# Kernel optimization log

Measured on AMD Instinct MI355X. Metric: run time of the kernel, lower is better.

## Reference

```python
import jax, jax.numpy as jnp
import numpy as np

EPS = 1e-12  # torch F.normalize eps
K = 32       # num_clusters (hardcoded in module)

def l2norm(v, axis):
    n = jnp.sqrt(jnp.sum(v * v, axis=axis, keepdims=True))
    return v / jnp.maximum(n, EPS)

def setup_inputs() -> dict:
    key = jax.random.key(0)
    k1, k2, k3, k4 = jax.random.split(key, 4)
    B, M, D = 64, 128, 2048
    x = jax.random.normal(k1, (B, M, D), dtype=jnp.float32)
    # ragged lengths in [1, M]
    lengths = jax.random.randint(k2, (B,), 0, M, dtype=jnp.int32) + 1
    init_sc = 1.0 / np.sqrt(D)
    W = init_sc * jax.random.normal(k3, (K, D), dtype=jnp.float32)  # fc1.weight
    C = init_sc * jax.random.normal(k4, (K, D), dtype=jnp.float32)  # centroids
    return {"x": x, "lengths": lengths, "W": W, "C": C}

def reference(x, lengths, W, C):
    # x: [B,M,D] padded frames, lengths: [B] valid frame counts
    B, M, D = x.shape
    mask = (jnp.arange(M)[None, :] < lengths[:, None]).astype(x.dtype)  # [B,M]
    cnt = lengths.astype(x.dtype)[:, None]                              # [B,1]
    # avg pooling over valid (raw, un-normalized) frames
    avgpool = jnp.sum(x * mask[:, :, None], axis=1) / cnt               # [B,D]
    # per-frame L2 normalize
    xn = l2norm(x, axis=-1)                                             # [B,M,D]
    # soft assignment: linear (no bias) + softmax over clusters
    logits = jnp.einsum('bmd,kd->bmk', xn, W)
    a = jax.nn.softmax(logits, axis=-1) * mask[:, :, None]              # [B,M,K]
    # VLAD residual aggregation, GEMM form:
    # sum_m a[b,m,k]*(xn[b,m,:] - C[k,:]) = (a^T xn) - C * sum_m a
    ax = jnp.einsum('bmk,bmd->bkd', a, xn)                              # [B,K,D]
    asum = jnp.sum(a, axis=1)                                           # [B,K]
    vlad = ax - asum[:, :, None] * C[None, :, :]                        # [B,K,D]
    # intra-normalize per cluster, flatten, global L2 normalize
    vlad = l2norm(vlad, axis=2)
    vlad = vlad.reshape(B, K * D)
    vlad = l2norm(vlad, axis=1)
    return jnp.concatenate([avgpool, vlad], axis=1)                     # [B, D + K*D]
```

## Files before the change

### kernel.cpp

```cpp
#include <hip/hip_runtime.h>
#include <math.h>

#define BB 64
#define MM 128
#define DDIM 2048
#define KK 32
#define NDC 16
#define OUTROW (DDIM + KK*DDIM)

typedef __attribute__((ext_vector_type(8))) short bf16x8;
typedef __attribute__((ext_vector_type(4))) float f32x4;

__device__ __forceinline__ short f2bf(float f) {
  unsigned u = __builtin_bit_cast(unsigned, f);
  u += 0x7fffu + ((u >> 16) & 1u);
  return (short)(u >> 16);
}
__device__ __forceinline__ unsigned pack2(float lo, float hi) {
  return (unsigned)(unsigned short)f2bf(lo) | ((unsigned)(unsigned short)f2bf(hi) << 16);
}

__global__ __launch_bounds__(256) void k_prep(const float* __restrict__ W,
                                              short* __restrict__ Wb) {
  int i = (blockIdx.x * 256 + threadIdx.x) * 8;
  float4 a = *(const float4*)(W + i);
  float4 b = *(const float4*)(W + i + 4);
  bf16x8 o = {f2bf(a.x), f2bf(a.y), f2bf(a.z), f2bf(a.w),
              f2bf(b.x), f2bf(b.y), f2bf(b.z), f2bf(b.w)};
  *(bf16x8*)(Wb + i) = o;
}

__global__ __launch_bounds__(256, 4) void k_logits(const float* __restrict__ x,
    const int* __restrict__ lengths, const short* __restrict__ Wb,
    short* __restrict__ aT, float* __restrict__ asum_p) {
  const int t = threadIdx.x, wv = t >> 6, lane = t & 63;
  const int l15 = lane & 15, quad = lane >> 4;
  const int fg = blockIdx.x;
  const int g0 = fg * 16;
  const int b  = fg >> 3;
  const int m0 = (fg & 7) * 16;
  const int len = lengths[b];

  if (m0 >= len) {
    if (t < KK) asum_p[(size_t)fg * KK + t] = 0.f;
    const int zk = t >> 3, zoff = (t & 7) * 2;
    *(unsigned*)(aT + (size_t)b * KK * MM + (size_t)zk * MM + m0 + zoff) = 0u;
    return;
  }

  const bool av = (m0 + l15) < len;
  const float* xrow = x + (size_t)(g0 + l15) * DDIM + wv * 512 + quad * 8;
  const short* w0   = Wb + l15 * DDIM + wv * 512 + quad * 8;
  const short* w1   = w0 + 16 * DDIM;

  f32x4 c0 = {0.f, 0.f, 0.f, 0.f}, c1 = {0.f, 0.f, 0.f, 0.f};
  float ssq = 0.f;
  #pragma unroll
  for (int h = 0; h < 4; ++h) {
    float4 xa[4], xc[4];
    bf16x8 B0[4], B1[4];
    #pragma unroll
    for (int s = 0; s < 4; ++s) {
      const int so = h * 4 + s;
      if (av) {
        xa[s] = *(const float4*)(xrow + so * 32);
        xc[s] = *(const float4*)(xrow + so * 32 + 4);
      } else {
        xa[s] = make_float4(0.f, 0.f, 0.f, 0.f);
        xc[s] = make_float4(0.f, 0.f, 0.f, 0.f);
      }
      B0[s] = *(const bf16x8*)(w0 + so * 32);
      B1[s] = *(const bf16x8*)(w1 + so * 32);
    }
    #pragma unroll
    for (int s = 0; s < 4; ++s) {
      ssq = fmaf(xa[s].x, xa[s].x, ssq); ssq = fmaf(xa[s].y, xa[s].y, ssq);
      ssq = fmaf(xa[s].z, xa[s].z, ssq); ssq = fmaf(xa[s].w, xa[s].w, ssq);
      ssq = fmaf(xc[s].x, xc[s].x, ssq); ssq = fmaf(xc[s].y, xc[s].y, ssq);
      ssq = fmaf(xc[s].z, xc[s].z, ssq); ssq = fmaf(xc[s].w, xc[s].w, ssq);
      bf16x8 A = {f2bf(xa[s].x), f2bf(xa[s].y), f2bf(xa[s].z), f2bf(xa[s].w),
                  f2bf(xc[s].x), f2bf(xc[s].y), f2bf(xc[s].z), f2bf(xc[s].w)};
      c0 = __builtin_amdgcn_mfma_f32_16x16x32_bf16(A, B0[s], c0, 0, 0, 0);
      c1 = __builtin_amdgcn_mfma_f32_16x16x32_bf16(A, B1[s], c1, 0, 0, 0);
    }
  }

  ssq += __shfl_xor(ssq, 16, 64);
  ssq += __shfl_xor(ssq, 32, 64);
  __shared__ float sq[4][16];
  __shared__ float lg[4][16][33];
  if (quad == 0) sq[wv][l15] = ssq;
  #pragma unroll
  for (int r = 0; r < 4; ++r) {
    lg[wv][quad * 4 + r][l15]      = c0[r];
    lg[wv][quad * 4 + r][16 + l15] = c1[r];
  }
  __syncthreads();

  const int fr = t >> 4, kk = (t & 15) * 2;
  float s0 = 0.f, s1 = 0.f;
  #pragma unroll
  for (int w = 0; w < 4; ++w) { s0 += lg[w][fr][kk]; s1 += lg[w][fr][kk + 1]; }
  float ss  = sq[0][fr] + sq[1][fr] + sq[2][fr] + sq[3][fr];
  float inv = 1.f / fmaxf(sqrtf(ss), 1e-12f);
  s0 *= inv; s1 *= inv;
  float mx = fmaxf(s0, s1);
  mx = fmaxf(mx, __shfl_xor(mx, 1, 64));
  mx = fmaxf(mx, __shfl_xor(mx, 2, 64));
  mx = fmaxf(mx, __shfl_xor(mx, 4, 64));
  mx = fmaxf(mx, __shfl_xor(mx, 8, 64));
  float e0 = __expf(s0 - mx), e1 = __expf(s1 - mx);
  float se = e0 + e1;
  se += __shfl_xor(se, 1, 64);
  se += __shfl_xor(se, 2, 64);
  se += __shfl_xor(se, 4, 64);
  se += __shfl_xor(se, 8, 64);
  const bool valid = (m0 + fr) < len;
  float rr = valid ? (1.f / se) : 0.f;
  float a0 = e0 * rr, a1 = e1 * rr;

  __syncthreads();
  lg[0][fr][kk] = a0; lg[0][fr][kk + 1] = a1;
  __syncthreads();
  if (t < KK) {
    float s = 0.f;
    #pragma unroll
    for (int f = 0; f < 16; ++f) s += lg[0][f][t];
    asum_p[(size_t)fg * KK + t] = s;
  }
  short* ap = aT + (size_t)b * KK * MM + m0 + fr;
  ap[(size_t)kk * MM]       = f2bf(a0 * inv);
  ap[(size_t)(kk + 1) * MM] = f2bf(a1 * inv);
}

__global__ __launch_bounds__(256, 4) void k_vlad(const float* __restrict__ x,
    const int* __restrict__ lengths, const float* __restrict__ Cc,
    const short* __restrict__ aT, const float* __restrict__ asum_p,
    float* __restrict__ out, float* __restrict__ ssq_part) {
  const int t = threadIdx.x, wv = t >> 6, lane = t & 63;
  const int l15 = lane & 15, quad = lane >> 4;
  const int dc = blockIdx.x, b = blockIdx.y;
  const int dh = wv & 1, mh = wv >> 1;
  const int dwb = dc * 128 + dh * 64;
  const int mb  = mh * 64;
  const int len = lengths[b];

  __shared__ __attribute__((aligned(16))) char ubuf[20480];
  short (*xbt)[64][40]     = (short(*)[64][40])ubuf;
  float (*exch)[2][64][20] = (float(*)[2][64][20])ubuf;
  __shared__ float  asl[KK];
  __shared__ float4 avp[2][16];
  __shared__ float  ssw[4][17];

  if (t < KK) {
    float s = 0.f;
    #pragma unroll
    for (int p = 0; p < 8; ++p) s += asum_p[(size_t)(b * 8 + p) * KK + t];
    asl[t] = s;
  }

  const float* xb  = x  + (size_t)b * MM * DDIM;
  const short* at0 = aT + (size_t)b * KK * MM + l15 * MM + mb + quad * 8;

  const int q4   = l15 * 4;
  const int mrow = quad * 2;
  const int keyw = l15 & 3;
  const int keyr = (l15 >> 2) & 3;

  bf16x8 A0[2], A1[2];
  #pragma unroll
  for (int ms = 0; ms < 2; ++ms) {
    A0[ms] = *(const bf16x8*)(at0 + ms * 32);
    A1[ms] = *(const bf16x8*)(at0 + 16 * MM + ms * 32);
  }

  float4 v0[8], v1[8];
  #pragma unroll
  for (int ms = 0; ms < 2; ++ms) {
    #pragma unroll
    for (int p = 0; p < 4; ++p) {
      const int m = mb + ms * 32 + p * 8 + mrow;
      const float* xr = xb + (size_t)m * DDIM + dwb + q4;
      v0[ms * 4 + p] = (m < len) ? *(const float4*)xr
                                 : make_float4(0.f, 0.f, 0.f, 0.f);
      v1[ms * 4 + p] = (m + 1 < len) ? *(const float4*)(xr + DDIM)
                                     : make_float4(0.f, 0.f, 0.f, 0.f);
    }
  }

  float avg[4] = {0.f, 0.f, 0.f, 0.f};
  #pragma unroll
  for (int i = 0; i < 8; ++i) {
    avg[0] += v0[i].x + v1[i].x;
    avg[1] += v0[i].y + v1[i].y;
    avg[2] += v0[i].z + v1[i].z;
    avg[3] += v0[i].w + v1[i].w;
  }
  #pragma unroll
  for (int c = 0; c < 4; ++c) {
    avg[c] += __shfl_xor(avg[c], 16, 64);
    avg[c] += __shfl_xor(avg[c], 32, 64);
  }
  if (mh == 1 && quad == 0)
    avp[dh][l15] = make_float4(avg[0], avg[1], avg[2], avg[3]);

  f32x4 acc0[4], acc1[4];
  #pragma unroll
  for (int nt = 0; nt < 4; ++nt) {
    acc0[nt] = (f32x4){0.f, 0.f, 0.f, 0.f};
    acc1[nt] = (f32x4){0.f, 0.f, 0.f, 0.f};
  }

  #pragma unroll
  for (int ms = 0; ms < 2; ++ms) {
    #pragma unroll
    for (int p = 0; p < 4; ++p) {
      const int i = ms * 4 + p;
      const int mls = (p ^ keyw) * 8 + mrow;
      *(unsigned*)&xbt[wv][q4 + 0][mls] = pack2(v0[i].x, v1[i].x);
      *(unsigned*)&xbt[wv][q4 + 1][mls] = pack2(v0[i].y, v1[i].y);
      *(unsigned*)&xbt[wv][q4 + 2][mls] = pack2(v0[i].z, v1[i].z);
      *(unsigned*)&xbt[wv][q4 + 3][mls] = pack2(v0[i].w, v1[i].w);
    }
    #pragma unroll
    for (int nt = 0; nt < 4; ++nt) {
      bf16x8 B = *(const bf16x8*)&xbt[wv][nt * 16 + l15][(quad ^ keyr) * 8];
      acc0[nt] = __builtin_amdgcn_mfma_f32_16x16x32_bf16(A0[ms], B, acc0[nt], 0, 0, 0);
      acc1[nt] = __builtin_amdgcn_mfma_f32_16x16x32_bf16(A1[ms], B, acc1[nt], 0, 0, 0);
    }
  }

  f32x4 keep[4], give[4];
  if (mh == 0) {
    #pragma unroll
    for (int nt = 0; nt < 4; ++nt) { keep[nt] = acc0[nt]; give[nt] = acc1[nt]; }
  } else {
    #pragma unroll
    for (int nt = 0; nt < 4; ++nt) { keep[nt] = acc1[nt]; give[nt] = acc0[nt]; }
  }

  __syncthreads();
  #pragma unroll
  for (int nt = 0; nt < 4; ++nt)
    *(f32x4*)&exch[dh][mh][lane][nt * 4] = give[nt];

  if (mh == 0 && quad == 0) {
    float4 pa = avp[dh][l15];
    float rl = 1.f / (float)len;
    *(float4*)(out + (size_t)b * OUTROW + dwb + q4) =
        make_float4((avg[0] + pa.x) * rl, (avg[1] + pa.y) * rl,
                    (avg[2] + pa.z) * rl, (avg[3] + pa.w) * rl);
  }

  __syncthreads();
  #pragma unroll
  for (int nt = 0; nt < 4; ++nt)
    keep[nt] += *(const f32x4*)&exch[dh][1 - mh][lane][nt * 4];

  float* orow = out + (size_t)b * OUTROW + DDIM;
  #pragma unroll
  for (int r = 0; r < 4; ++r) {
    const int k = mh * 16 + quad * 4 + r;
    const float as = asl[k];
    float sqv = 0.f;
    #pragma unroll
    for (int nt = 0; nt < 4; ++nt) {
      const int d = dwb + nt * 16 + l15;
      float v = keep[nt][r] - as * Cc[(size_t)k * DDIM + d];
      orow[(size_t)k * DDIM + d] = v;
      sqv = fmaf(v, v, sqv);
    }
    sqv += __shfl_xor(sqv, 1, 64);
    sqv += __shfl_xor(sqv, 2, 64);
    sqv += __shfl_xor(sqv, 4, 64);
    sqv += __shfl_xor(sqv, 8, 64);
    if (l15 == 0) ssw[wv][quad * 4 + r] = sqv;
  }
  __syncthreads();
  if (t < KK) {
    const int mt = t >> 4, kl = t & 15;
    ssq_part[((size_t)dc * BB + b) * KK + t] = ssw[mt * 2][kl] + ssw[mt * 2 + 1][kl];
  }
}

__global__ __launch_bounds__(256) void k_norm(const float* __restrict__ ssq_part,
    float* __restrict__ out) {
  const int t = threadIdx.x;
  const int k = blockIdx.x;
  const int b = blockIdx.y;
  __shared__ float ssk[32];
  if (t < 32) {
    float sk = 0.f;
    #pragma unroll
    for (int dc = 0; dc < NDC; ++dc)
      sk += ssq_part[((size_t)dc * BB + b) * KK + t];
    ssk[t] = sk;
  }
  __syncthreads();
  float gss = 0.f, iv_own = 0.f;
  #pragma unroll
  for (int kk = 0; kk < 32; ++kk) {
    float nk = sqrtf(ssk[kk]);
    float iv = 1.f / fmaxf(nk, 1e-12f);
    float nn = nk * iv;
    gss += nn * nn;
    if (kk == k) iv_own = iv;
  }
  float sc = iv_own / fmaxf(sqrtf(gss), 1e-12f);
  float* row = out + (size_t)b * OUTROW + DDIM + (size_t)k * DDIM;
  #pragma unroll
  for (int h = 0; h < 2; ++h) {
    float4* p = (float4*)(row + h * 1024 + t * 4);
    float4 v = *p;
    v.x *= sc; v.y *= sc; v.z *= sc; v.w *= sc;
    *p = v;
  }
}

extern "C" void kernel_launch(void* const* d_in, const int* in_sizes, int n_in,
                              void* d_out, int out_size, void* d_ws, size_t ws_size,
                              hipStream_t stream) {
  const float* x       = (const float*)d_in[0];
  const int*   lengths = (const int*)d_in[1];
  const float* W       = (const float*)d_in[2];
  const float* C       = (const float*)d_in[3];
  float* out = (float*)d_out;

  short* Wb     = (short*)d_ws;
  short* aT     = Wb + (size_t)KK * DDIM;
  float* asum_p = (float*)(aT + (size_t)BB * KK * MM);
  float* ssqp   = asum_p + (size_t)512 * KK;

  k_prep  <<<dim3(32),      256, 0, stream>>>(W, Wb);
  k_logits<<<dim3(512),     256, 0, stream>>>(x, lengths, Wb, aT, asum_p);
  k_vlad  <<<dim3(NDC, BB), 256, 0, stream>>>(x, lengths, C, aT, asum_p, out, ssqp);
  k_norm  <<<dim3(KK, BB),  256, 0, stream>>>(ssqp, out);
}
```

Before: 158.1 us.

## Stage x and W tiles through LDS in logits kernel, drop W prep kernel

```diff
diff --git a/kernel.cpp b/kernel.cpp
--- a/kernel.cpp
+++ b/kernel.cpp
@@ -20,18 +20,8 @@
   return (unsigned)(unsigned short)f2bf(lo) | ((unsigned)(unsigned short)f2bf(hi) << 16);
 }
 
-__global__ __launch_bounds__(256) void k_prep(const float* __restrict__ W,
-                                              short* __restrict__ Wb) {
-  int i = (blockIdx.x * 256 + threadIdx.x) * 8;
-  float4 a = *(const float4*)(W + i);
-  float4 b = *(const float4*)(W + i + 4);
-  bf16x8 o = {f2bf(a.x), f2bf(a.y), f2bf(a.z), f2bf(a.w),
-              f2bf(b.x), f2bf(b.y), f2bf(b.z), f2bf(b.w)};
-  *(bf16x8*)(Wb + i) = o;
-}
-
-__global__ __launch_bounds__(256, 4) void k_logits(const float* __restrict__ x,
-    const int* __restrict__ lengths, const short* __restrict__ Wb,
+__global__ __launch_bounds__(256, 2) void k_logits(const float* __restrict__ x,
+    const int* __restrict__ lengths, const float* __restrict__ W,
     short* __restrict__ aT, float* __restrict__ asum_p) {
   const int t = threadIdx.x, wv = t >> 6, lane = t & 63;
   const int l15 = lane & 15, quad = lane >> 4;
@@ -48,48 +38,71 @@
     return;
   }
 
-  const bool av = (m0 + l15) < len;
-  const float* xrow = x + (size_t)(g0 + l15) * DDIM + wv * 512 + quad * 8;
-  const short* w0   = Wb + l15 * DDIM + wv * 512 + quad * 8;
-  const short* w1   = w0 + 16 * DDIM;
-
+  __shared__ short xs[16][520];
+  __shared__ short ws[32][520];
+  __shared__ float sqf[16];
+  __shared__ float lg[4][16][33];
+
+  const int xr = t >> 4;
+  const int xc = (t & 15) * 8;
+  const bool rv = (m0 + xr) < len;
+  const float* xrow = x + (size_t)(g0 + xr) * DDIM;
+  const int wr = t >> 3;
+  const int wc = (t & 7) * 8;
+  const float* wrow = W + (size_t)wr * DDIM;
+
+  float ssq = 0.f;
   f32x4 c0 = {0.f, 0.f, 0.f, 0.f}, c1 = {0.f, 0.f, 0.f, 0.f};
-  float ssq = 0.f;
+
   #pragma unroll
   for (int h = 0; h < 4; ++h) {
-    float4 xa[4], xc[4];
-    bf16x8 B0[4], B1[4];
+    const int d0 = h * 512;
+    #pragma unroll
+    for (int p = 0; p < 4; ++p) {
+      const int col = p * 128 + xc;
+      float4 a, c;
+      if (rv) {
+        a = *(const float4*)(xrow + d0 + col);
+        c = *(const float4*)(xrow + d0 + col + 4);
+      } else {
+        a = make_float4(0.f, 0.f, 0.f, 0.f);
+        c = make_float4(0.f, 0.f, 0.f, 0.f);
+      }
+      ssq = fmaf(a.x, a.x, ssq); ssq = fmaf(a.y, a.y, ssq);
+      ssq = fmaf(a.z, a.z, ssq); ssq = fmaf(a.w, a.w, ssq);
+      ssq = fmaf(c.x, c.x, ssq); ssq = fmaf(c.y, c.y, ssq);
+      ssq = fmaf(c.z, c.z, ssq); ssq = fmaf(c.w, c.w, ssq);
+      bf16x8 o = {f2bf(a.x), f2bf(a.y), f2bf(a.z), f2bf(a.w),
+                  f2bf(c.x), f2bf(c.y), f2bf(c.z), f2bf(c.w)};
+      *(bf16x8*)&xs[xr][col] = o;
+    }
+    #pragma unroll
+    for (int p = 0; p < 8; ++p) {
+      const int col = p * 64 + wc;
+      float4 a = *(const float4*)(wrow + d0 + col);
+      float4 c = *(const float4*)(wrow + d0 + col + 4);
+      bf16x8 o = {f2bf(a.x), f2bf(a.y), f2bf(a.z), f2bf(a.w),
+                  f2bf(c.x), f2bf(c.y), f2bf(c.z), f2bf(c.w)};
+      *(bf16x8*)&ws[wr][col] = o;
+    }
+    __syncthreads();
     #pragma unroll
     for (int s = 0; s < 4; ++s) {
-      const int so = h * 4 + s;
-      if (av) {
-        xa[s] = *(const float4*)(xrow + so * 32);
-        xc[s] = *(const float4*)(xrow + so * 32 + 4);
-      } else {
-        xa[s] = make_float4(0.f, 0.f, 0.f, 0.f);
-        xc[s] = make_float4(0.f, 0.f, 0.f, 0.f);
-      }
-      B0[s] = *(const bf16x8*)(w0 + so * 32);
-      B1[s] = *(const bf16x8*)(w1 + so * 32);
-    }
-    #pragma unroll
-    for (int s = 0; s < 4; ++s) {
-      ssq = fmaf(xa[s].x, xa[s].x, ssq); ssq = fmaf(xa[s].y, xa[s].y, ssq);
-      ssq = fmaf(xa[s].z, xa[s].z, ssq); ssq = fmaf(xa[s].w, xa[s].w, ssq);
-      ssq = fmaf(xc[s].x, xc[s].x, ssq); ssq = fmaf(xc[s].y, xc[s].y, ssq);
-      ssq = fmaf(xc[s].z, xc[s].z, ssq); ssq = fmaf(xc[s].w, xc[s].w, ssq);
-      bf16x8 A = {f2bf(xa[s].x), f2bf(xa[s].y), f2bf(xa[s].z), f2bf(xa[s].w),
-                  f2bf(xc[s].x), f2bf(xc[s].y), f2bf(xc[s].z), f2bf(xc[s].w)};
-      c0 = __builtin_amdgcn_mfma_f32_16x16x32_bf16(A, B0[s], c0, 0, 0, 0);
-      c1 = __builtin_amdgcn_mfma_f32_16x16x32_bf16(A, B1[s], c1, 0, 0, 0);
-    }
-  }
-
-  ssq += __shfl_xor(ssq, 16, 64);
-  ssq += __shfl_xor(ssq, 32, 64);
-  __shared__ float sq[4][16];
-  __shared__ float lg[4][16][33];
-  if (quad == 0) sq[wv][l15] = ssq;
+      const int off = wv * 128 + s * 32 + quad * 8;
+      bf16x8 A  = *(const bf16x8*)&xs[l15][off];
+      bf16x8 B0 = *(const bf16x8*)&ws[l15][off];
+      bf16x8 B1 = *(const bf16x8*)&ws[16 + l15][off];
+      c0 = __builtin_amdgcn_mfma_f32_16x16x32_bf16(A, B0, c0, 0, 0, 0);
+      c1 = __builtin_amdgcn_mfma_f32_16x16x32_bf16(A, B1, c1, 0, 0, 0);
+    }
+    __syncthreads();
+  }
+
+  ssq += __shfl_xor(ssq, 1, 64);
+  ssq += __shfl_xor(ssq, 2, 64);
+  ssq += __shfl_xor(ssq, 4, 64);
+  ssq += __shfl_xor(ssq, 8, 64);
+  if ((lane & 15) == 0) sqf[xr] = ssq;
   #pragma unroll
   for (int r = 0; r < 4; ++r) {
     lg[wv][quad * 4 + r][l15]      = c0[r];
@@ -101,7 +114,7 @@
   float s0 = 0.f, s1 = 0.f;
   #pragma unroll
   for (int w = 0; w < 4; ++w) { s0 += lg[w][fr][kk]; s1 += lg[w][fr][kk + 1]; }
-  float ss  = sq[0][fr] + sq[1][fr] + sq[2][fr] + sq[3][fr];
+  float ss  = sqf[fr];
   float inv = 1.f / fmaxf(sqrtf(ss), 1e-12f);
   s0 *= inv; s1 *= inv;
   float mx = fmaxf(s0, s1);
@@ -326,13 +339,11 @@
   const float* C       = (const float*)d_in[3];
   float* out = (float*)d_out;
 
-  short* Wb     = (short*)d_ws;
-  short* aT     = Wb + (size_t)KK * DDIM;
+  short* aT     = (short*)d_ws;
   float* asum_p = (float*)(aT + (size_t)BB * KK * MM);
   float* ssqp   = asum_p + (size_t)512 * KK;
 
-  k_prep  <<<dim3(32),      256, 0, stream>>>(W, Wb);
-  k_logits<<<dim3(512),     256, 0, stream>>>(x, lengths, Wb, aT, asum_p);
+  k_logits<<<dim3(512),     256, 0, stream>>>(x, lengths, W, aT, asum_p);
   k_vlad  <<<dim3(NDC, BB), 256, 0, stream>>>(x, lengths, C, aT, asum_p, out, ssqp);
   k_norm  <<<dim3(KK, BB),  256, 0, stream>>>(ssqp, out);
 }
```

New measurement: 139.6 us (median of 2 runs). 1.13x faster.
